# Optimization experiments

Hardware: AMD Instinct MI355X
Metric: run time of the kernel (lower is better)

The kernel has to match this reference:

```python
import jax, jax.numpy as jnp
import numpy as np

B, L, H = 4, 96, 512
R, T = 257, 21


def setup_inputs() -> dict:
    key = jax.random.key(0)
    ks = jax.random.split(key, 7)
    std_in = (2.0 / (H + 1 + R)) ** 0.5  # xavier_normal over [H+1, R]
    return {
        "layer1": jax.random.normal(ks[0], (B, L, H), jnp.float32),
        "layer2": jax.random.normal(ks[1], (B, L, H), jnp.float32),
        "layer3": jax.random.normal(ks[2], (B, L, H), jnp.float32),
        "W_1": jax.random.normal(ks[3], (H + 1, R), jnp.float32) * std_in,
        "W_2": jax.random.normal(ks[4], (H + 1, R), jnp.float32) * std_in,
        "W_3": jax.random.normal(ks[5], (H + 1, R), jnp.float32) * std_in,
        "W_l": jax.random.normal(ks[6], (1, R, T), jnp.float32),
    }


def reference(layer1, layer2, layer3, W_1, W_2, W_3, W_l):
    # Append bias-ones feature, as in the torch forward.
    ones = jnp.ones((*layer1.shape[:2], 1), layer1.dtype)
    l1 = jnp.concatenate([layer1, ones], axis=-1)  # [n, i, H+1]
    l2 = jnp.concatenate([layer2, ones], axis=-1)  # [n, j, H+1]
    l3 = jnp.concatenate([layer3, jnp.ones((*layer3.shape[:-1], 1), layer3.dtype)], axis=-1)
    # Factor the CP contraction: project each stream to rank space first.
    p1 = jnp.einsum("nia,ar->nir", l1, W_1)  # [n, i, r]
    p2 = jnp.einsum("njb,br->njr", l2, W_2)  # [n, j, r]
    p3 = jnp.einsum("nkc,cr->nkr", l3, W_3)  # [n, k, r]
    # Fold label map into one stream, then rank-reduce outer product.
    p3t = jnp.einsum("nkr,rt->ntkr", p3, W_l[0])  # [n, t, k, r]
    out = jnp.einsum("nir,njr,ntkr->ntijk", p1, p2, p3t)  # [n, t, i, j, k]
    return out
```

## Files before the change

### kernel.cpp

```cpp
#include <hip/hip_runtime.h>
#include <hip/hip_bf16.h>

#define RR 257
#define RP 288
#define TT 21

typedef __attribute__((ext_vector_type(4))) float f32x4;
typedef __attribute__((ext_vector_type(8))) short bf16x8;

union Pack8 { unsigned short s[8]; uint4 v; };

__device__ __forceinline__ unsigned short f2b(float f) {
    union { float f; unsigned u; } v; v.f = f;
    unsigned r = v.u + 0x7fffu + ((v.u >> 16) & 1u);
    return (unsigned short)(r >> 16);
}

__global__ __launch_bounds__(384) void proj_kernel(
    const float* __restrict__ l1, const float* __restrict__ l2, const float* __restrict__ l3,
    const float* __restrict__ W1, const float* __restrict__ W2, const float* __restrict__ W3,
    float* __restrict__ P1f, float* __restrict__ P2f, float* __restrict__ P3f)
{
    int bx = blockIdx.x;
    int grp = bx % 24;
    int n = (bx / 24) & 3;
    int s = bx / 96;
    const float* layer = (s == 0) ? l1 : (s == 1) ? l2 : l3;
    const float* W     = (s == 0) ? W1 : (s == 1) ? W2 : W3;
    int i0 = grp * 4;

    __shared__ __attribute__((aligned(16))) float x[2048];
    const float4* src = (const float4*)(layer + (n * 96 + i0) * 512);
    float4* xv = (float4*)x;
    for (int idx = threadIdx.x; idx < 512; idx += 384) xv[idx] = src[idx];
    __syncthreads();

    int r = threadIdx.x;
    if (r < RP) {
        float a0 = 0.f, a1 = 0.f, a2 = 0.f, a3 = 0.f;
        if (r < RR) {
            float b = W[512 * RR + r];
            a0 = a1 = a2 = a3 = b;
            #pragma unroll 8
            for (int a = 0; a < 512; ++a) {
                float wa = W[a * RR + r];
                a0 = fmaf(x[a], wa, a0);
                a1 = fmaf(x[512 + a], wa, a1);
                a2 = fmaf(x[1024 + a], wa, a2);
                a3 = fmaf(x[1536 + a], wa, a3);
            }
        }
        float* P = (s == 0) ? P1f : (s == 1) ? P2f : P3f;
        int base = (n * 96 + i0) * RP + r;
        P[base]          = a0;
        P[base + RP]     = a1;
        P[base + 2 * RP] = a2;
        P[base + 3 * RP] = a3;
    }
}

__global__ __launch_bounds__(256) void aprep_kernel(
    const float* __restrict__ P1f, const float* __restrict__ P2f,
    unsigned short* __restrict__ Af)
{
    int bx = blockIdx.x;
    int n = bx / 96, i = bx % 96;
    __shared__ __attribute__((aligned(16))) float p1row[RP];
    for (int r = threadIdx.x; r < RP; r += 256)
        p1row[r] = P1f[(n * 96 + i) * RP + r];
    __syncthreads();

    unsigned short* dst = Af + (size_t)(n * 576 + i * 6) * 9 * 512;
    for (int idx = threadIdx.x; idx < 3456; idx += 256) {
        int L = idx & 63;
        int rest = idx >> 6;
        int ks = rest % 9, rgl = rest / 9;
        int j = rgl * 16 + (L & 15);
        int k8 = ks * 32 + (L >> 4) * 8;
        const float* p2p = P2f + (n * 96 + j) * RP + k8;
        float4 b0 = *(const float4*)(p2p);
        float4 b1 = *(const float4*)(p2p + 4);
        float4 a0 = *(const float4*)(p1row + k8);
        float4 a1 = *(const float4*)(p1row + k8 + 4);
        Pack8 u;
        u.s[0] = f2b(a0.x * b0.x); u.s[1] = f2b(a0.y * b0.y);
        u.s[2] = f2b(a0.z * b0.z); u.s[3] = f2b(a0.w * b0.w);
        u.s[4] = f2b(a1.x * b1.x); u.s[5] = f2b(a1.y * b1.y);
        u.s[6] = f2b(a1.z * b1.z); u.s[7] = f2b(a1.w * b1.w);
        *(uint4*)(dst + (size_t)(rgl * 9 + ks) * 512 + L * 8) = u.v;
    }
}

__global__ __launch_bounds__(256) void bprep_kernel(
    const float* __restrict__ P3f, const float* __restrict__ Wl,
    unsigned short* __restrict__ Bf)
{
    int bx = blockIdx.x;
    int h = bx & 1;
    int t = (bx >> 1) % TT, n = bx / (2 * TT);
    __shared__ __attribute__((aligned(16))) float wl_lds[RP];
    for (int r = threadIdx.x; r < RP; r += 256)
        wl_lds[r] = (r < RR) ? Wl[r * TT + t] : 0.f;
    __syncthreads();

    unsigned short* dst = Bf + (size_t)(n * TT + t) * 6 * 9 * 512;
    for (int idx2 = threadIdx.x; idx2 < 1728; idx2 += 256) {
        int idx = h * 1728 + idx2;
        int L = idx & 63;
        int rest = idx >> 6;
        int ks = rest % 9, kg = rest / 9;
        int col = kg * 16 + (L & 15);
        int r8 = ks * 32 + (L >> 4) * 8;
        const float* p3p = P3f + (n * 96 + col) * RP + r8;
        float4 p0 = *(const float4*)(p3p);
        float4 p1 = *(const float4*)(p3p + 4);
        float4 w0 = *(const float4*)(wl_lds + r8);
        float4 w1 = *(const float4*)(wl_lds + r8 + 4);
        Pack8 u;
        u.s[0] = f2b(p0.x * w0.x); u.s[1] = f2b(p0.y * w0.y);
        u.s[2] = f2b(p0.z * w0.z); u.s[3] = f2b(p0.w * w0.w);
        u.s[4] = f2b(p1.x * w1.x); u.s[5] = f2b(p1.y * w1.y);
        u.s[6] = f2b(p1.z * w1.z); u.s[7] = f2b(p1.w * w1.w);
        *(uint4*)(dst + (size_t)(kg * 9 + ks) * 512 + L * 8) = u.v;
    }
}

#define LOADA(s, kss) { _Pragma("unroll") for (int mf = 0; mf < 6; ++mf) \
    fa[s][mf] = *(const bf16x8*)(abase + (mf * 9 + (kss)) * 512); }
#define LOADB(kss) { _Pragma("unroll") for (int nf = 0; nf < 6; ++nf) \
    fb[nf] = *(const bf16x8*)(lbase + (nf * 9 + (kss)) * 512); }
#define MFMAS(s) { _Pragma("unroll") for (int nf = 0; nf < 6; ++nf) { \
    _Pragma("unroll") for (int mf = 0; mf < 6; ++mf) \
      acc[mf][nf] = __builtin_amdgcn_mfma_f32_16x16x32_bf16(fb[nf], fa[s][mf], acc[mf][nf], 0, 0, 0); } }

__global__ __launch_bounds__(256, 2) void tri9_kernel(
    const unsigned short* __restrict__ Af, const unsigned short* __restrict__ Bf,
    float* __restrict__ out)
{
    int orig = blockIdx.x;
    int bx = (orig & 7) * 252 + (orig >> 3);
    int t = bx % TT;
    int mtn = bx / TT;
    int mt = mtn % 24;
    int n = mtn / 24;

    int tid = threadIdx.x, lane = tid & 63, wv = tid >> 6;

    __shared__ __attribute__((aligned(16))) unsigned short blds[27648];

    {
        const uint4* bsrc = (const uint4*)(Bf + (size_t)(n * TT + t) * 27648);
        uint4* bdst = (uint4*)blds;
        for (int idx = tid; idx < 3456; idx += 256) bdst[idx] = bsrc[idx];
    }
    __syncthreads();

    const unsigned short* abase =
        Af + (size_t)(n * 576 + mt * 24 + wv * 6) * 9 * 512 + lane * 8;
    const unsigned short* lbase = blds + lane * 8;

    f32x4 acc[6][6] = {};
    bf16x8 fa[2][6], fb[6];

    LOADA(0, 0);
    #pragma unroll
    for (int ks = 0; ks < 9; ++ks) {
        if (ks < 8) {
            if (ks & 1) { LOADA(0, ks + 1); } else { LOADA(1, ks + 1); }
        }
        LOADB(ks);
        if (ks & 1) { MFMAS(1); } else { MFMAS(0); }
    }

    __syncthreads();
    float* tb = (float*)blds + wv * 1600;
    int Llo = lane & 15, Lhi = lane >> 4;
    size_t outbase = ((size_t)(n * TT + t) * 9216 + mt * 384 + wv * 96) * 96;

    #pragma unroll
    for (int mf = 0; mf < 6; ++mf) {
        #pragma unroll
        for (int nf = 0; nf < 6; ++nf)
            *(f32x4*)&tb[Llo * 100 + nf * 16 + Lhi * 4] = acc[mf][nf];
        float* gdst = out + outbase + (size_t)mf * 16 * 96;
        #pragma unroll
        for (int q = 0; q < 6; ++q) {
            int fidx = q * 64 + lane;
            int ml = fidx / 24, k4 = fidx % 24;
            f32x4 vv = *(const f32x4*)&tb[ml * 100 + k4 * 4];
            *(f32x4*)(gdst + (size_t)fidx * 4) = vv;
        }
    }
}

extern "C" void kernel_launch(void* const* d_in, const int* in_sizes, int n_in,
                              void* d_out, int out_size, void* d_ws, size_t ws_size,
                              hipStream_t stream) {
    const float* l1 = (const float*)d_in[0];
    const float* l2 = (const float*)d_in[1];
    const float* l3 = (const float*)d_in[2];
    const float* W1 = (const float*)d_in[3];
    const float* W2 = (const float*)d_in[4];
    const float* W3 = (const float*)d_in[5];
    const float* Wl = (const float*)d_in[6];

    float* P1f = (float*)d_ws;
    float* P2f = P1f + 384 * RP;
    float* P3f = P2f + 384 * RP;
    unsigned short* Af = (unsigned short*)(P3f + 384 * RP);
    unsigned short* Bf = Af + (size_t)4 * 576 * 9 * 512;

    proj_kernel<<<288, 384, 0, stream>>>(l1, l2, l3, W1, W2, W3, P1f, P2f, P3f);
    aprep_kernel<<<384, 256, 0, stream>>>(P1f, P2f, Af);
    bprep_kernel<<<168, 256, 0, stream>>>(P3f, Wl, Bf);
    tri9_kernel<<<2016, 256, 0, stream>>>(Af, Bf, (float*)d_out);
}
```

Measured before the change: 123.5 us.

## Merge prep kernels, halve projection rows per block, store MFMA outputs directly

The projection kernel now handles two rows per block instead of four, doubling its grid to 576 blocks for more parallelism at the cost of more weight reloads. The A and B prep kernels are fused into one launch, dividing work by block index, which saves one kernel launch. The main MFMA kernel swaps operand order so each lane holds four consecutive rows of one column and writes them straight to global memory, dropping the LDS transpose staging and its barrier. The direct stores are scalar 4-byte writes with a row stride, which may coalesce worse than the previous 16-byte vector writes.

```diff
diff --git a/kernel.cpp b/kernel.cpp
--- a/kernel.cpp
+++ b/kernel.cpp
@@ -22,106 +22,100 @@
     float* __restrict__ P1f, float* __restrict__ P2f, float* __restrict__ P3f)
 {
     int bx = blockIdx.x;
-    int grp = bx % 24;
-    int n = (bx / 24) & 3;
-    int s = bx / 96;
+    int grp = bx % 48;
+    int n = (bx / 48) & 3;
+    int s = bx / 192;
     const float* layer = (s == 0) ? l1 : (s == 1) ? l2 : l3;
     const float* W     = (s == 0) ? W1 : (s == 1) ? W2 : W3;
-    int i0 = grp * 4;
-
-    __shared__ __attribute__((aligned(16))) float x[2048];
+    int i0 = grp * 2;
+
+    __shared__ __attribute__((aligned(16))) float x[1024];
     const float4* src = (const float4*)(layer + (n * 96 + i0) * 512);
     float4* xv = (float4*)x;
-    for (int idx = threadIdx.x; idx < 512; idx += 384) xv[idx] = src[idx];
+    for (int idx = threadIdx.x; idx < 256; idx += 384) xv[idx] = src[idx];
     __syncthreads();
 
     int r = threadIdx.x;
     if (r < RP) {
-        float a0 = 0.f, a1 = 0.f, a2 = 0.f, a3 = 0.f;
+        float a0 = 0.f, a1 = 0.f;
         if (r < RR) {
             float b = W[512 * RR + r];
-            a0 = a1 = a2 = a3 = b;
+            a0 = a1 = b;
             #pragma unroll 8
             for (int a = 0; a < 512; ++a) {
                 float wa = W[a * RR + r];
                 a0 = fmaf(x[a], wa, a0);
                 a1 = fmaf(x[512 + a], wa, a1);
-                a2 = fmaf(x[1024 + a], wa, a2);
-                a3 = fmaf(x[1536 + a], wa, a3);
             }
         }
         float* P = (s == 0) ? P1f : (s == 1) ? P2f : P3f;
         int base = (n * 96 + i0) * RP + r;
-        P[base]          = a0;
-        P[base + RP]     = a1;
-        P[base + 2 * RP] = a2;
-        P[base + 3 * RP] = a3;
-    }
-}
-
-__global__ __launch_bounds__(256) void aprep_kernel(
+        P[base]      = a0;
+        P[base + RP] = a1;
+    }
+}
+
+__global__ __launch_bounds__(256) void prep_kernel(
     const float* __restrict__ P1f, const float* __restrict__ P2f,
-    unsigned short* __restrict__ Af)
+    const float* __restrict__ P3f, const float* __restrict__ Wl,
+    unsigned short* __restrict__ Af, unsigned short* __restrict__ Bf)
 {
     int bx = blockIdx.x;
-    int n = bx / 96, i = bx % 96;
-    __shared__ __attribute__((aligned(16))) float p1row[RP];
-    for (int r = threadIdx.x; r < RP; r += 256)
-        p1row[r] = P1f[(n * 96 + i) * RP + r];
-    __syncthreads();
-
-    unsigned short* dst = Af + (size_t)(n * 576 + i * 6) * 9 * 512;
-    for (int idx = threadIdx.x; idx < 3456; idx += 256) {
-        int L = idx & 63;
-        int rest = idx >> 6;
-        int ks = rest % 9, rgl = rest / 9;
-        int j = rgl * 16 + (L & 15);
-        int k8 = ks * 32 + (L >> 4) * 8;
-        const float* p2p = P2f + (n * 96 + j) * RP + k8;
-        float4 b0 = *(const float4*)(p2p);
-        float4 b1 = *(const float4*)(p2p + 4);
-        float4 a0 = *(const float4*)(p1row + k8);
-        float4 a1 = *(const float4*)(p1row + k8 + 4);
-        Pack8 u;
-        u.s[0] = f2b(a0.x * b0.x); u.s[1] = f2b(a0.y * b0.y);
-        u.s[2] = f2b(a0.z * b0.z); u.s[3] = f2b(a0.w * b0.w);
-        u.s[4] = f2b(a1.x * b1.x); u.s[5] = f2b(a1.y * b1.y);
-        u.s[6] = f2b(a1.z * b1.z); u.s[7] = f2b(a1.w * b1.w);
-        *(uint4*)(dst + (size_t)(rgl * 9 + ks) * 512 + L * 8) = u.v;
-    }
-}
-
-__global__ __launch_bounds__(256) void bprep_kernel(
-    const float* __restrict__ P3f, const float* __restrict__ Wl,
-    unsigned short* __restrict__ Bf)
-{
-    int bx = blockIdx.x;
-    int h = bx & 1;
-    int t = (bx >> 1) % TT, n = bx / (2 * TT);
-    __shared__ __attribute__((aligned(16))) float wl_lds[RP];
-    for (int r = threadIdx.x; r < RP; r += 256)
-        wl_lds[r] = (r < RR) ? Wl[r * TT + t] : 0.f;
-    __syncthreads();
-
-    unsigned short* dst = Bf + (size_t)(n * TT + t) * 6 * 9 * 512;
-    for (int idx2 = threadIdx.x; idx2 < 1728; idx2 += 256) {
-        int idx = h * 1728 + idx2;
-        int L = idx & 63;
-        int rest = idx >> 6;
-        int ks = rest % 9, kg = rest / 9;
-        int col = kg * 16 + (L & 15);
-        int r8 = ks * 32 + (L >> 4) * 8;
-        const float* p3p = P3f + (n * 96 + col) * RP + r8;
-        float4 p0 = *(const float4*)(p3p);
-        float4 p1 = *(const float4*)(p3p + 4);
-        float4 w0 = *(const float4*)(wl_lds + r8);
-        float4 w1 = *(const float4*)(wl_lds + r8 + 4);
-        Pack8 u;
-        u.s[0] = f2b(p0.x * w0.x); u.s[1] = f2b(p0.y * w0.y);
-        u.s[2] = f2b(p0.z * w0.z); u.s[3] = f2b(p0.w * w0.w);
-        u.s[4] = f2b(p1.x * w1.x); u.s[5] = f2b(p1.y * w1.y);
-        u.s[6] = f2b(p1.z * w1.z); u.s[7] = f2b(p1.w * w1.w);
-        *(uint4*)(dst + (size_t)(kg * 9 + ks) * 512 + L * 8) = u.v;
+    if (bx < 384) {
+        int n = bx / 96, i = bx % 96;
+        __shared__ __attribute__((aligned(16))) float p1row[RP];
+        for (int r = threadIdx.x; r < RP; r += 256)
+            p1row[r] = P1f[(n * 96 + i) * RP + r];
+        __syncthreads();
+
+        unsigned short* dst = Af + (size_t)(n * 576 + i * 6) * 9 * 512;
+        for (int idx = threadIdx.x; idx < 3456; idx += 256) {
+            int L = idx & 63;
+            int rest = idx >> 6;
+            int ks = rest % 9, rgl = rest / 9;
+            int j = rgl * 16 + (L & 15);
+            int k8 = ks * 32 + (L >> 4) * 8;
+            const float* p2p = P2f + (n * 96 + j) * RP + k8;
+            float4 b0 = *(const float4*)(p2p);
+            float4 b1 = *(const float4*)(p2p + 4);
+            float4 a0 = *(const float4*)(p1row + k8);
+            float4 a1 = *(const float4*)(p1row + k8 + 4);
+            Pack8 u;
+            u.s[0] = f2b(a0.x * b0.x); u.s[1] = f2b(a0.y * b0.y);
+            u.s[2] = f2b(a0.z * b0.z); u.s[3] = f2b(a0.w * b0.w);
+            u.s[4] = f2b(a1.x * b1.x); u.s[5] = f2b(a1.y * b1.y);
+            u.s[6] = f2b(a1.z * b1.z); u.s[7] = f2b(a1.w * b1.w);
+            *(uint4*)(dst + (size_t)(rgl * 9 + ks) * 512 + L * 8) = u.v;
+        }
+    } else {
+        int b2 = bx - 384;
+        int h = b2 & 1;
+        int t = (b2 >> 1) % TT, n = b2 / (2 * TT);
+        __shared__ __attribute__((aligned(16))) float wl_lds[RP];
+        for (int r = threadIdx.x; r < RP; r += 256)
+            wl_lds[r] = (r < RR) ? Wl[r * TT + t] : 0.f;
+        __syncthreads();
+
+        unsigned short* dst = Bf + (size_t)(n * TT + t) * 6 * 9 * 512;
+        for (int idx2 = threadIdx.x; idx2 < 1728; idx2 += 256) {
+            int idx = h * 1728 + idx2;
+            int L = idx & 63;
+            int rest = idx >> 6;
+            int ks = rest % 9, kg = rest / 9;
+            int col = kg * 16 + (L & 15);
+            int r8 = ks * 32 + (L >> 4) * 8;
+            const float* p3p = P3f + (n * 96 + col) * RP + r8;
+            float4 p0 = *(const float4*)(p3p);
+            float4 p1 = *(const float4*)(p3p + 4);
+            float4 w0 = *(const float4*)(wl_lds + r8);
+            float4 w1 = *(const float4*)(wl_lds + r8 + 4);
+            Pack8 u;
+            u.s[0] = f2b(p0.x * w0.x); u.s[1] = f2b(p0.y * w0.y);
+            u.s[2] = f2b(p0.z * w0.z); u.s[3] = f2b(p0.w * w0.w);
+            u.s[4] = f2b(p1.x * w1.x); u.s[5] = f2b(p1.y * w1.y);
+            u.s[6] = f2b(p1.z * w1.z); u.s[7] = f2b(p1.w * w1.w);
+            *(uint4*)(dst + (size_t)(kg * 9 + ks) * 512 + L * 8) = u.v;
+        }
     }
 }
 
@@ -131,9 +125,9 @@
     fb[nf] = *(const bf16x8*)(lbase + (nf * 9 + (kss)) * 512); }
 #define MFMAS(s) { _Pragma("unroll") for (int nf = 0; nf < 6; ++nf) { \
     _Pragma("unroll") for (int mf = 0; mf < 6; ++mf) \
-      acc[mf][nf] = __builtin_amdgcn_mfma_f32_16x16x32_bf16(fb[nf], fa[s][mf], acc[mf][nf], 0, 0, 0); } }
-
-__global__ __launch_bounds__(256, 2) void tri9_kernel(
+      acc[mf][nf] = __builtin_amdgcn_mfma_f32_16x16x32_bf16(fa[s][mf], fb[nf], acc[mf][nf], 0, 0, 0); } }
+
+__global__ __launch_bounds__(256, 2) void tri11_kernel(
     const unsigned short* __restrict__ Af, const unsigned short* __restrict__ Bf,
     float* __restrict__ out)
 {
@@ -172,23 +166,19 @@
         if (ks & 1) { MFMAS(1); } else { MFMAS(0); }
     }
 
-    __syncthreads();
-    float* tb = (float*)blds + wv * 1600;
-    int Llo = lane & 15, Lhi = lane >> 4;
     size_t outbase = ((size_t)(n * TT + t) * 9216 + mt * 384 + wv * 96) * 96;
+    int kcol = lane & 15;
+    int mrow0 = (lane >> 4) * 4;
 
     #pragma unroll
     for (int mf = 0; mf < 6; ++mf) {
+        float* rowp = out + outbase + (size_t)(mf * 16 + mrow0) * 96 + kcol;
         #pragma unroll
-        for (int nf = 0; nf < 6; ++nf)
-            *(f32x4*)&tb[Llo * 100 + nf * 16 + Lhi * 4] = acc[mf][nf];
-        float* gdst = out + outbase + (size_t)mf * 16 * 96;
-        #pragma unroll
-        for (int q = 0; q < 6; ++q) {
-            int fidx = q * 64 + lane;
-            int ml = fidx / 24, k4 = fidx % 24;
-            f32x4 vv = *(const f32x4*)&tb[ml * 100 + k4 * 4];
-            *(f32x4*)(gdst + (size_t)fidx * 4) = vv;
+        for (int nf = 0; nf < 6; ++nf) {
+            float* gp = rowp + nf * 16;
+            #pragma unroll
+            for (int v = 0; v < 4; ++v)
+                gp[(size_t)v * 96] = acc[mf][nf][v];
         }
     }
 }
@@ -210,8 +200,7 @@
     unsigned short* Af = (unsigned short*)(P3f + 384 * RP);
     unsigned short* Bf = Af + (size_t)4 * 576 * 9 * 512;
 
-    proj_kernel<<<288, 384, 0, stream>>>(l1, l2, l3, W1, W2, W3, P1f, P2f, P3f);
-    aprep_kernel<<<384, 256, 0, stream>>>(P1f, P2f, Af);
-    bprep_kernel<<<168, 256, 0, stream>>>(P3f, Wl, Bf);
-    tri9_kernel<<<2016, 256, 0, stream>>>(Af, Bf, (float*)d_out);
-}
+    proj_kernel<<<576, 384, 0, stream>>>(l1, l2, l3, W1, W2, W3, P1f, P2f, P3f);
+    prep_kernel<<<552, 256, 0, stream>>>(P1f, P2f, P3f, Wl, Af, Bf);
+    tri11_kernel<<<2016, 256, 0, stream>>>(Af, Bf, (float*)d_out);
+}
```

Result: faster. 118.4 us (-4.1%).
